# Kernel optimization log

Hardware: AMD Instinct MI355X
Metric: run time of the kernel (lower is better)

Reference implementation:

```python
import jax, jax.numpy as jnp
import numpy as np
from jax import lax

WINDOW_SIZE = 9
MAX_DISP = 192
RADIUS = WINDOW_SIZE // 2


def setup_inputs() -> dict:
    key = jax.random.key(0)
    k1, k2, k3 = jax.random.split(key, 3)
    B, H, W = 2, 256, 512
    left_img = jax.random.uniform(k1, (B, 1, H, W), dtype=jnp.float32)
    right_img = jax.random.uniform(k2, (B, 1, H, W), dtype=jnp.float32)
    target_disp = jax.random.randint(k3, (B, 1, H, W), 0, MAX_DISP).astype(jnp.float32)
    return {"left_img": left_img, "right_img": right_img, "target_disp": target_disp}


def _census_transform(img):
    # img: [B,1,H,W] -> census bits: [B, ws*ws-1, H-2r, W-2r]
    # (original allocates ws*ws channels but leaves the center-slot channel
    #  all-zero; it contributes 0 to the hamming sum, so we omit it.)
    B, _, H, W = img.shape
    Hc, Wc = H - 2 * RADIUS, W - 2 * RADIUS
    center = img[:, :, RADIUS:RADIUS + Hc, RADIUS:RADIUS + Wc]
    chans = []
    for i in range(WINDOW_SIZE):
        for j in range(WINDOW_SIZE):
            if i == RADIUS and j == RADIUS:
                continue
            win = img[:, :, i:i + Hc, j:j + Wc]
            chans.append((win > center).astype(jnp.float32))
    return jnp.concatenate(chans, axis=1)  # [B, 80, Hc, Wc]


def _cost_volume(left_census, right_census):
    # hamming cost per disparity via scan (one [B,1,Hc,Wc] slice at a time)
    Wc = left_census.shape[-1]
    w_base = jnp.arange(Wc)

    def step(carry, d):
        widx = w_base + d
        valid = (widx < Wc)[None, None, None, :]
        rc_d = jnp.where(valid,
                         right_census[..., jnp.clip(widx, 0, Wc - 1)],
                         jnp.float32(0))
        cost = jnp.sum(jnp.abs(left_census - rc_d), axis=1, keepdims=True)
        return carry, cost  # [B,1,Hc,Wc]

    _, costs = lax.scan(step, None, jnp.arange(MAX_DISP))  # [D,B,1,Hc,Wc]
    return jnp.moveaxis(costs, 0, 2)  # [B,1,D,Hc,Wc]


def reference(left_img, right_img, target_disp):
    lc = _census_transform(left_img)
    rc = _census_transform(right_img)
    cost_volume = _cost_volume(lc, rc)  # [B,1,D,Hc,Wc]

    disp_crop = target_disp[:, :, RADIUS:-RADIUS, RADIUS:-RADIUS]  # [B,1,Hc,Wc]
    tidx = jnp.clip(disp_crop.astype(jnp.int32), 0, MAX_DISP - 1)
    # gather cost at target disparity per pixel
    best_cost = jnp.take_along_axis(cost_volume, tidx[:, :, None], axis=2)[:, :, 0]
    mask = (disp_crop > 0).astype(jnp.float32)
    valid_pixels = jnp.sum(mask) + 1e-6
    return jnp.sum(best_cost * mask) / valid_pixels
```

## Files before the change

### kernel.cpp

```cpp
#include <hip/hip_runtime.h>

constexpr int RADIUS   = 4;
constexpr int MAX_DISP = 192;
constexpr int B  = 2;
constexpr int H  = 256;
constexpr int W  = 512;
constexpr int Hc = H - 2 * RADIUS;
constexpr int Wc = W - 2 * RADIUS;
constexpr int TOTAL = B * Hc * Wc;

constexpr int BLOCK = 256;
constexpr int GRID  = (TOTAL + BLOCK - 1) / BLOCK;

__device__ __forceinline__ void census80(const float* __restrict__ base,
                                         int cy, int cx,
                                         unsigned long long& lo,
                                         unsigned long long& hi) {
    const float c = base[cy * W + cx];
    unsigned long long l = 0, h = 0;
    int bit = 0;
    #pragma unroll
    for (int i = -RADIUS; i <= RADIUS; ++i) {
        #pragma unroll
        for (int j = -RADIUS; j <= RADIUS; ++j) {
            if (i == 0 && j == 0) continue;
            const unsigned long long t =
                (base[(cy + i) * W + (cx + j)] > c) ? 1ull : 0ull;
            if (bit < 64) l |= t << bit;
            else          h |= t << (bit - 64);
            ++bit;
        }
    }
    lo = l; hi = h;
}

__global__ __launch_bounds__(BLOCK)
void fused_kernel(const float* __restrict__ left,
                  const float* __restrict__ right,
                  const float* __restrict__ disp,
                  uint2* __restrict__ partials) {
    const int idx = blockIdx.x * BLOCK + threadIdx.x;

    unsigned int cost = 0, cnt = 0;
    if (idx < TOTAL) {
        const int x = idx % Wc;
        const int r = idx / Wc;
        const int y = r % Hc;
        const int b = r / Hc;

        const float dval = disp[((size_t)b * H + (y + RADIUS)) * W + (x + RADIUS)];
        if (dval > 0.0f) {
            cnt = 1;
            const int d = min((int)dval, MAX_DISP - 1);

            const float* lb = left  + (size_t)b * H * W;
            const float* rb = right + (size_t)b * H * W;

            unsigned long long llo, lhi;
            census80(lb, y + RADIUS, x + RADIUS, llo, lhi);

            if (x + d < Wc) {
                unsigned long long rlo, rhi;
                census80(rb, y + RADIUS, x + d + RADIUS, rlo, rhi);
                cost = (unsigned int)(__popcll(llo ^ rlo) + __popcll(lhi ^ rhi));
            } else {
                cost = (unsigned int)(__popcll(llo) + __popcll(lhi));
            }
        }
    }

    #pragma unroll
    for (int off = 32; off > 0; off >>= 1) {
        cost += __shfl_down(cost, off);
        cnt  += __shfl_down(cnt,  off);
    }

    __shared__ uint2 lds[BLOCK / 64];
    const int wave = threadIdx.x >> 6;
    if ((threadIdx.x & 63) == 0) lds[wave] = make_uint2(cost, cnt);
    __syncthreads();

    if (threadIdx.x == 0) {
        unsigned int c = 0, n = 0;
        #pragma unroll
        for (int w = 0; w < BLOCK / 64; ++w) { c += lds[w].x; n += lds[w].y; }
        partials[blockIdx.x] = make_uint2(c, n);
    }
}

__global__ __launch_bounds__(BLOCK)
void reduce_kernel(const uint2* __restrict__ partials,
                   float* __restrict__ out) {
    unsigned int c = 0, n = 0;
    for (int i = threadIdx.x; i < GRID; i += BLOCK) {
        const uint2 p = partials[i];
        c += p.x; n += p.y;
    }
    #pragma unroll
    for (int off = 32; off > 0; off >>= 1) {
        c += __shfl_down(c, off);
        n += __shfl_down(n, off);
    }
    __shared__ uint2 lds[BLOCK / 64];
    const int wave = threadIdx.x >> 6;
    if ((threadIdx.x & 63) == 0) lds[wave] = make_uint2(c, n);
    __syncthreads();
    if (threadIdx.x == 0) {
        unsigned int tc = 0, tn = 0;
        #pragma unroll
        for (int w = 0; w < BLOCK / 64; ++w) { tc += lds[w].x; tn += lds[w].y; }
        out[0] = (float)tc / ((float)tn + 1e-6f);
    }
}

extern "C" void kernel_launch(void* const* d_in, const int* in_sizes, int n_in,
                              void* d_out, int out_size, void* d_ws, size_t ws_size,
                              hipStream_t stream) {
    const float* left  = (const float*)d_in[0];
    const float* right = (const float*)d_in[1];
    const float* disp  = (const float*)d_in[2];
    float* out = (float*)d_out;
    uint2* partials = (uint2*)d_ws;

    fused_kernel<<<GRID, BLOCK, 0, stream>>>(left, right, disp, partials);
    reduce_kernel<<<1, BLOCK, 0, stream>>>(partials, out);
}
```

Measured before the change: 73.51 us.

## Precompute census bit tables for both images, then gather in separate loss kernel

Splits the fused kernel into a census kernel that writes 80-bit census codes for every pixel of both images into workspace, and a loss kernel that gathers left and right codes at the target disparity. The census kernel handles 4 adjacent pixels per thread with float4 row loads, so overlapping window reads are shared. This avoids computing two full 80-tap census windows per pixel from global memory. In exchange it adds an extra kernel launch and about 8 MB of table writes and reads, and it falls back to the old path if the workspace is too small.

Result: faster. 71.08 us (-3.3%).

```diff
diff --git a/kernel.cpp b/kernel.cpp
--- a/kernel.cpp
+++ b/kernel.cpp
@@ -10,76 +10,214 @@
 constexpr int TOTAL = B * Hc * Wc;
 
 constexpr int BLOCK = 256;
-constexpr int GRID  = (TOTAL + BLOCK - 1) / BLOCK;
-
-__device__ __forceinline__ void census80(const float* __restrict__ base,
-                                         int cy, int cx,
-                                         unsigned long long& lo,
-                                         unsigned long long& hi) {
+
+constexpr int TX   = 4;
+constexpr int TPR  = Wc / TX;
+constexpr int NROWS = 2 * B * Hc;
+constexpr int CENSUS_THREADS = NROWS * TPR;
+constexpr int CENSUS_GRID = (CENSUS_THREADS + BLOCK - 1) / BLOCK;
+
+constexpr int LOSS_THREADS = TOTAL / TX;
+constexpr int LOSS_GRID = (LOSS_THREADS + BLOCK - 1) / BLOCK;
+
+constexpr size_t PARTIALS_OFF = 0;
+constexpr size_t TAB_OFF      = 4096;
+constexpr size_t TAB_ELEMS    = (size_t)2 * B * Hc * Wc;
+constexpr size_t WS_NEEDED    = TAB_OFF + TAB_ELEMS * sizeof(ulonglong2);
+
+__global__ __launch_bounds__(BLOCK)
+void census_kernel(const float* __restrict__ left,
+                   const float* __restrict__ right,
+                   ulonglong2* __restrict__ tab) {
+    const int tid = blockIdx.x * BLOCK + threadIdx.x;
+    if (tid >= CENSUS_THREADS) return;
+
+    const int t   = tid % TPR;
+    const int row = tid / TPR;
+    const int x0  = t * TX;
+    const int y   = row % Hc;
+    const int ib  = row / Hc;
+    const int b   = ib % B;
+    const int img = ib / B;
+
+    const float* base = (img ? right : left)
+                        + (size_t)b * H * W + (size_t)y * W + x0;
+
+    float f[9][12];
+    #pragma unroll
+    for (int r = 0; r < 9; ++r) {
+        const float4* p = (const float4*)(base + r * W);
+        const float4 a = p[0], m = p[1], c = p[2];
+        f[r][0]=a.x; f[r][1]=a.y; f[r][2]=a.z;  f[r][3]=a.w;
+        f[r][4]=m.x; f[r][5]=m.y; f[r][6]=m.z;  f[r][7]=m.w;
+        f[r][8]=c.x; f[r][9]=c.y; f[r][10]=c.z; f[r][11]=c.w;
+    }
+
+    const float ctr[TX] = { f[4][4], f[4][5], f[4][6], f[4][7] };
+    unsigned long long lo[TX] = {0,0,0,0};
+    unsigned long long hi[TX] = {0,0,0,0};
+
+    #pragma unroll
+    for (int r = 0; r < 9; ++r) {
+        #pragma unroll
+        for (int j = 0; j < 9; ++j) {
+            if (r == 4 && j == 4) continue;
+            const int bit = r * 9 + j;
+            #pragma unroll
+            for (int p = 0; p < TX; ++p) {
+                const unsigned long long tb = (f[r][p + j] > ctr[p]) ? 1ull : 0ull;
+                if (bit < 64) lo[p] |= tb << bit;
+                else          hi[p] |= tb << (bit - 64);
+            }
+        }
+    }
+
+    ulonglong2* o = tab + ((size_t)ib * Hc + y) * Wc + x0;
+    #pragma unroll
+    for (int p = 0; p < TX; ++p) {
+        ulonglong2 v; v.x = lo[p]; v.y = hi[p];
+        o[p] = v;
+    }
+}
+
+__global__ __launch_bounds__(BLOCK)
+void loss_kernel(const ulonglong2* __restrict__ tab,
+                 const float* __restrict__ disp,
+                 uint2* __restrict__ partials) {
+    const int tid = blockIdx.x * BLOCK + threadIdx.x;
+
+    unsigned int cost = 0, cnt = 0;
+    if (tid < LOSS_THREADS) {
+        const int t   = tid % TPR;
+        const int row = tid / TPR;
+        const int x0  = t * TX;
+        const int y   = row % Hc;
+        const int b   = row / Hc;
+
+        const float4 d4 = *(const float4*)(disp + ((size_t)b * H + y + RADIUS) * W
+                                                + x0 + RADIUS);
+        const float dv[TX] = { d4.x, d4.y, d4.z, d4.w };
+
+        const ulonglong2* lrow = tab + ((size_t)b * Hc + y) * Wc;
+        const ulonglong2* rrow = tab + ((size_t)(B + b) * Hc + y) * Wc;
+
+        #pragma unroll
+        for (int p = 0; p < TX; ++p) {
+            if (dv[p] > 0.0f) {
+                ++cnt;
+                const int x = x0 + p;
+                const int d = min((int)dv[p], MAX_DISP - 1);
+                const ulonglong2 L = lrow[x];
+                if (x + d < Wc) {
+                    const ulonglong2 R = rrow[x + d];
+                    cost += (unsigned int)(__popcll(L.x ^ R.x) + __popcll(L.y ^ R.y));
+                } else {
+                    cost += (unsigned int)(__popcll(L.x) + __popcll(L.y));
+                }
+            }
+        }
+    }
+
+    #pragma unroll
+    for (int off = 32; off > 0; off >>= 1) {
+        cost += __shfl_down(cost, off);
+        cnt  += __shfl_down(cnt,  off);
+    }
+
+    __shared__ uint2 lds[BLOCK / 64];
+    const int wave = threadIdx.x >> 6;
+    if ((threadIdx.x & 63) == 0) lds[wave] = make_uint2(cost, cnt);
+    __syncthreads();
+
+    if (threadIdx.x == 0) {
+        unsigned int c = 0, n = 0;
+        #pragma unroll
+        for (int w = 0; w < BLOCK / 64; ++w) { c += lds[w].x; n += lds[w].y; }
+        partials[blockIdx.x] = make_uint2(c, n);
+    }
+}
+
+__global__ __launch_bounds__(BLOCK)
+void reduce_kernel(const uint2* __restrict__ partials,
+                   float* __restrict__ out) {
+    unsigned int c = 0, n = 0;
+    for (int i = threadIdx.x; i < LOSS_GRID; i += BLOCK) {
+        const uint2 p = partials[i];
+        c += p.x; n += p.y;
+    }
+    #pragma unroll
+    for (int off = 32; off > 0; off >>= 1) {
+        c += __shfl_down(c, off);
+        n += __shfl_down(n, off);
+    }
+    __shared__ uint2 lds[BLOCK / 64];
+    const int wave = threadIdx.x >> 6;
+    if ((threadIdx.x & 63) == 0) lds[wave] = make_uint2(c, n);
+    __syncthreads();
+    if (threadIdx.x == 0) {
+        unsigned int tc = 0, tn = 0;
+        #pragma unroll
+        for (int w = 0; w < BLOCK / 64; ++w) { tc += lds[w].x; tn += lds[w].y; }
+        out[0] = (float)tc / ((float)tn + 1e-6f);
+    }
+}
+
+constexpr int FGRID = (TOTAL + BLOCK - 1) / BLOCK;
+
+__device__ __forceinline__ void census80_direct(const float* __restrict__ base,
+                                                int cy, int cx,
+                                                unsigned long long& lo,
+                                                unsigned long long& hi) {
     const float c = base[cy * W + cx];
     unsigned long long l = 0, h = 0;
     int bit = 0;
     #pragma unroll
-    for (int i = -RADIUS; i <= RADIUS; ++i) {
+    for (int i = -RADIUS; i <= RADIUS; ++i)
         #pragma unroll
         for (int j = -RADIUS; j <= RADIUS; ++j) {
             if (i == 0 && j == 0) continue;
-            const unsigned long long t =
-                (base[(cy + i) * W + (cx + j)] > c) ? 1ull : 0ull;
-            if (bit < 64) l |= t << bit;
-            else          h |= t << (bit - 64);
+            const unsigned long long t = (base[(cy + i) * W + (cx + j)] > c) ? 1ull : 0ull;
+            if (bit < 64) l |= t << bit; else h |= t << (bit - 64);
             ++bit;
         }
-    }
     lo = l; hi = h;
 }
 
 __global__ __launch_bounds__(BLOCK)
-void fused_kernel(const float* __restrict__ left,
-                  const float* __restrict__ right,
-                  const float* __restrict__ disp,
-                  uint2* __restrict__ partials) {
+void fused_fallback(const float* __restrict__ left,
+                    const float* __restrict__ right,
+                    const float* __restrict__ disp,
+                    uint2* __restrict__ partials) {
     const int idx = blockIdx.x * BLOCK + threadIdx.x;
-
     unsigned int cost = 0, cnt = 0;
     if (idx < TOTAL) {
-        const int x = idx % Wc;
-        const int r = idx / Wc;
-        const int y = r % Hc;
-        const int b = r / Hc;
-
+        const int x = idx % Wc, y = (idx / Wc) % Hc, b = idx / (Wc * Hc);
         const float dval = disp[((size_t)b * H + (y + RADIUS)) * W + (x + RADIUS)];
         if (dval > 0.0f) {
             cnt = 1;
             const int d = min((int)dval, MAX_DISP - 1);
-
             const float* lb = left  + (size_t)b * H * W;
             const float* rb = right + (size_t)b * H * W;
-
             unsigned long long llo, lhi;
-            census80(lb, y + RADIUS, x + RADIUS, llo, lhi);
-
+            census80_direct(lb, y + RADIUS, x + RADIUS, llo, lhi);
             if (x + d < Wc) {
                 unsigned long long rlo, rhi;
-                census80(rb, y + RADIUS, x + d + RADIUS, rlo, rhi);
+                census80_direct(rb, y + RADIUS, x + d + RADIUS, rlo, rhi);
                 cost = (unsigned int)(__popcll(llo ^ rlo) + __popcll(lhi ^ rhi));
             } else {
                 cost = (unsigned int)(__popcll(llo) + __popcll(lhi));
             }
         }
     }
-
     #pragma unroll
     for (int off = 32; off > 0; off >>= 1) {
         cost += __shfl_down(cost, off);
         cnt  += __shfl_down(cnt,  off);
     }
-
     __shared__ uint2 lds[BLOCK / 64];
     const int wave = threadIdx.x >> 6;
     if ((threadIdx.x & 63) == 0) lds[wave] = make_uint2(cost, cnt);
     __syncthreads();
-
     if (threadIdx.x == 0) {
         unsigned int c = 0, n = 0;
         #pragma unroll
@@ -89,10 +227,9 @@
 }
 
 __global__ __launch_bounds__(BLOCK)
-void reduce_kernel(const uint2* __restrict__ partials,
-                   float* __restrict__ out) {
+void reduce_fallback(const uint2* __restrict__ partials, float* __restrict__ out) {
     unsigned int c = 0, n = 0;
-    for (int i = threadIdx.x; i < GRID; i += BLOCK) {
+    for (int i = threadIdx.x; i < FGRID; i += BLOCK) {
         const uint2 p = partials[i];
         c += p.x; n += p.y;
     }
@@ -120,8 +257,16 @@
     const float* right = (const float*)d_in[1];
     const float* disp  = (const float*)d_in[2];
     float* out = (float*)d_out;
-    uint2* partials = (uint2*)d_ws;
-
-    fused_kernel<<<GRID, BLOCK, 0, stream>>>(left, right, disp, partials);
-    reduce_kernel<<<1, BLOCK, 0, stream>>>(partials, out);
-}
+
+    if (ws_size >= WS_NEEDED) {
+        uint2*      partials = (uint2*)((char*)d_ws + PARTIALS_OFF);
+        ulonglong2* tab      = (ulonglong2*)((char*)d_ws + TAB_OFF);
+        census_kernel<<<CENSUS_GRID, BLOCK, 0, stream>>>(left, right, tab);
+        loss_kernel<<<LOSS_GRID, BLOCK, 0, stream>>>(tab, disp, partials);
+        reduce_kernel<<<1, BLOCK, 0, stream>>>(partials, out);
+    } else {
+        uint2* partials = (uint2*)d_ws;
+        fused_fallback<<<FGRID, BLOCK, 0, stream>>>(left, right, disp, partials);
+        reduce_fallback<<<1, BLOCK, 0, stream>>>(partials, out);
+    }
+}
```

## Compute right-row census once per block in LDS and tile four pixels per thread

Applied to the files above, without the earlier changes.

Each block now handles one output row. Half the threads compute the right-image census for the whole row into shared memory, and the other half compute the left census and look up the right descriptor at the target disparity from LDS. The old code recomputed a full 81-tap right census per pixel with scattered loads. Each thread now covers four adjacent pixels using float4 row loads, so neighbouring window values are shared across them. The cost is a block-wide sync and only half the threads doing cost accumulation.

Result: faster. 65.94 us (-10.3%).

```diff
diff --git a/kernel.cpp b/kernel.cpp
--- a/kernel.cpp
+++ b/kernel.cpp
@@ -7,64 +7,84 @@
 constexpr int W  = 512;
 constexpr int Hc = H - 2 * RADIUS;
 constexpr int Wc = W - 2 * RADIUS;
-constexpr int TOTAL = B * Hc * Wc;
 
 constexpr int BLOCK = 256;
-constexpr int GRID  = (TOTAL + BLOCK - 1) / BLOCK;
+constexpr int ROWS  = B * Hc;
+constexpr int TX    = 4;
+constexpr int TPR   = Wc / TX;
 
-__device__ __forceinline__ void census80(const float* __restrict__ base,
-                                         int cy, int cx,
-                                         unsigned long long& lo,
-                                         unsigned long long& hi) {
-    const float c = base[cy * W + cx];
-    unsigned long long l = 0, h = 0;
-    int bit = 0;
-    #pragma unroll
-    for (int i = -RADIUS; i <= RADIUS; ++i) {
+__global__ __launch_bounds__(BLOCK)
+void fused_row_kernel(const float* __restrict__ left,
+                      const float* __restrict__ right,
+                      const float* __restrict__ disp,
+                      uint2* __restrict__ partials) {
+    __shared__ ulonglong2 rbuf[Wc];
+    __shared__ uint2 red[BLOCK / 64];
+
+    const int bid = blockIdx.x;
+    const int b   = bid / Hc;
+    const int y   = bid % Hc;
+    const int tid = threadIdx.x;
+    const bool isRight = (tid < 128);
+    const int t   = tid & 127;
+    const int x0  = t * TX;
+
+    unsigned long long lo[TX] = {0,0,0,0};
+    unsigned long long hi[TX] = {0,0,0,0};
+
+    if (t < TPR) {
+        const float* img  = isRight ? right : left;
+        const float* base = img + ((size_t)b * H + y) * W + x0;
+
+        const float4 c4 = *(const float4*)(base + 4 * W + 4);
+        const float ctr[TX] = { c4.x, c4.y, c4.z, c4.w };
+
         #pragma unroll
-        for (int j = -RADIUS; j <= RADIUS; ++j) {
-            if (i == 0 && j == 0) continue;
-            const unsigned long long t =
-                (base[(cy + i) * W + (cx + j)] > c) ? 1ull : 0ull;
-            if (bit < 64) l |= t << bit;
-            else          h |= t << (bit - 64);
-            ++bit;
+        for (int r = 0; r < 9; ++r) {
+            const float4* p = (const float4*)(base + r * W);
+            const float4 a = p[0], m = p[1], cc = p[2];
+            const float f[12] = { a.x,a.y,a.z,a.w, m.x,m.y,m.z,m.w,
+                                  cc.x,cc.y,cc.z,cc.w };
+            #pragma unroll
+            for (int j = 0; j < 9; ++j) {
+                if (r == 4 && j == 4) continue;
+                const int bit = r * 9 + j;
+                #pragma unroll
+                for (int q = 0; q < TX; ++q) {
+                    const unsigned long long tb = (f[q + j] > ctr[q]) ? 1ull : 0ull;
+                    if (bit < 64) lo[q] |= tb << bit;
+                    else          hi[q] |= tb << (bit - 64);
+                }
+            }
+        }
+        if (isRight) {
+            #pragma unroll
+            for (int q = 0; q < TX; ++q) {
+                ulonglong2 v; v.x = lo[q]; v.y = hi[q];
+                rbuf[x0 + q] = v;
+            }
         }
     }
-    lo = l; hi = h;
-}
-
-__global__ __launch_bounds__(BLOCK)
-void fused_kernel(const float* __restrict__ left,
-                  const float* __restrict__ right,
-                  const float* __restrict__ disp,
-                  uint2* __restrict__ partials) {
-    const int idx = blockIdx.x * BLOCK + threadIdx.x;
+    __syncthreads();
 
     unsigned int cost = 0, cnt = 0;
-    if (idx < TOTAL) {
-        const int x = idx % Wc;
-        const int r = idx / Wc;
-        const int y = r % Hc;
-        const int b = r / Hc;
-
-        const float dval = disp[((size_t)b * H + (y + RADIUS)) * W + (x + RADIUS)];
-        if (dval > 0.0f) {
-            cnt = 1;
-            const int d = min((int)dval, MAX_DISP - 1);
-
-            const float* lb = left  + (size_t)b * H * W;
-            const float* rb = right + (size_t)b * H * W;
-
-            unsigned long long llo, lhi;
-            census80(lb, y + RADIUS, x + RADIUS, llo, lhi);
-
-            if (x + d < Wc) {
-                unsigned long long rlo, rhi;
-                census80(rb, y + RADIUS, x + d + RADIUS, rlo, rhi);
-                cost = (unsigned int)(__popcll(llo ^ rlo) + __popcll(lhi ^ rhi));
-            } else {
-                cost = (unsigned int)(__popcll(llo) + __popcll(lhi));
+    if (!isRight && t < TPR) {
+        const float4 d4 = *(const float4*)(disp + ((size_t)b * H + y + RADIUS) * W
+                                                + x0 + RADIUS);
+        const float dv[TX] = { d4.x, d4.y, d4.z, d4.w };
+        #pragma unroll
+        for (int q = 0; q < TX; ++q) {
+            if (dv[q] > 0.0f) {
+                ++cnt;
+                const int x = x0 + q;
+                const int d = min((int)dv[q], MAX_DISP - 1);
+                if (x + d < Wc) {
+                    const ulonglong2 R = rbuf[x + d];
+                    cost += (unsigned int)(__popcll(lo[q] ^ R.x) +
+                                           __popcll(hi[q] ^ R.y));
+                } else {
+                    cost += (unsigned int)(__popcll(lo[q]) + __popcll(hi[q]));
+                }
             }
         }
     }
@@ -74,17 +94,14 @@
         cost += __shfl_down(cost, off);
         cnt  += __shfl_down(cnt,  off);
     }
-
-    __shared__ uint2 lds[BLOCK / 64];
-    const int wave = threadIdx.x >> 6;
-    if ((threadIdx.x & 63) == 0) lds[wave] = make_uint2(cost, cnt);
+    const int wave = tid >> 6;
+    if ((tid & 63) == 0) red[wave] = make_uint2(cost, cnt);
     __syncthreads();
-
-    if (threadIdx.x == 0) {
+    if (tid == 0) {
         unsigned int c = 0, n = 0;
         #pragma unroll
-        for (int w = 0; w < BLOCK / 64; ++w) { c += lds[w].x; n += lds[w].y; }
-        partials[blockIdx.x] = make_uint2(c, n);
+        for (int w = 0; w < BLOCK / 64; ++w) { c += red[w].x; n += red[w].y; }
+        partials[bid] = make_uint2(c, n);
     }
 }
 
@@ -92,7 +109,7 @@
 void reduce_kernel(const uint2* __restrict__ partials,
                    float* __restrict__ out) {
     unsigned int c = 0, n = 0;
-    for (int i = threadIdx.x; i < GRID; i += BLOCK) {
+    for (int i = threadIdx.x; i < ROWS; i += BLOCK) {
         const uint2 p = partials[i];
         c += p.x; n += p.y;
     }
@@ -101,14 +118,14 @@
         c += __shfl_down(c, off);
         n += __shfl_down(n, off);
     }
-    __shared__ uint2 lds[BLOCK / 64];
+    __shared__ uint2 red[BLOCK / 64];
     const int wave = threadIdx.x >> 6;
-    if ((threadIdx.x & 63) == 0) lds[wave] = make_uint2(c, n);
+    if ((threadIdx.x & 63) == 0) red[wave] = make_uint2(c, n);
     __syncthreads();
     if (threadIdx.x == 0) {
         unsigned int tc = 0, tn = 0;
         #pragma unroll
-        for (int w = 0; w < BLOCK / 64; ++w) { tc += lds[w].x; tn += lds[w].y; }
+        for (int w = 0; w < BLOCK / 64; ++w) { tc += red[w].x; tn += red[w].y; }
         out[0] = (float)tc / ((float)tn + 1e-6f);
     }
 }
@@ -122,6 +139,6 @@
     float* out = (float*)d_out;
     uint2* partials = (uint2*)d_ws;
 
-    fused_kernel<<<GRID, BLOCK, 0, stream>>>(left, right, disp, partials);
+    fused_row_kernel<<<ROWS, BLOCK, 0, stream>>>(left, right, disp, partials);
     reduce_kernel<<<1, BLOCK, 0, stream>>>(partials, out);
 }
```
